# Performance work log

Measured on AMD Instinct MI355X. Metric: run time of the kernel, lower is better.

## Reference

```python
import jax, jax.numpy as jnp
import numpy as np

N_WIRES = 6
DIM = 1 << N_WIRES  # 64, equals input channel dim C for amplitude encoding
HID = N_WIRES       # hidden_dim = len(ops)


def _rx(theta):
    c = jnp.cos(theta / 2).astype(jnp.complex64)
    s = jnp.sin(theta / 2).astype(jnp.complex64)
    return jnp.stack([jnp.stack([c, -1j * s]), jnp.stack([-1j * s, c])])


def _ry(theta):
    c = jnp.cos(theta / 2).astype(jnp.complex64)
    s = jnp.sin(theta / 2).astype(jnp.complex64)
    return jnp.stack([jnp.stack([c, -s]), jnp.stack([s, c])])


def _apply_1q(state, U, wire):
    # state: (N, 2, 2, ..., 2); apply 2x2 U on qubit axis wire+1
    s = jnp.moveaxis(state, wire + 1, 1)
    s = jnp.einsum('ab,nb...->na...', U, s)
    return jnp.moveaxis(s, 1, wire + 1)


def _apply_cnot(state, c, t):
    # flip target axis where control bit == 1
    s = jnp.moveaxis(state, (c + 1, t + 1), (1, 2))
    s = jnp.concatenate([s[:, :1], jnp.flip(s[:, 1:2], axis=2)], axis=1)
    return jnp.moveaxis(s, (1, 2), (c + 1, t + 1))


def _expval_z(state, wire):
    # <Z_wire> = P(bit=0) - P(bit=1)
    p = state.real ** 2 + state.imag ** 2
    p = jnp.moveaxis(p, wire + 1, 1).reshape(p.shape[0], 2, -1)
    return p[:, 0].sum(-1) - p[:, 1].sum(-1)


def _value_layer(x_flat, params, qk):
    # amplitude encoding: normalize input into state amplitudes (C == DIM)
    norm = jnp.linalg.norm(x_flat, axis=-1, keepdims=True)
    psi = (x_flat / norm).astype(jnp.complex64)
    state = psi.reshape((x_flat.shape[0],) + (2,) * N_WIRES)
    rx0, ry0, ry1 = params[0], params[1], params[2]
    for j in range(N_WIRES):
        state = _apply_1q(state, _rx(rx0[j]), j)
        state = _apply_1q(state, _ry(ry0[j]), j)
    for j in range(N_WIRES):
        state = _apply_cnot(state, j, (j + 1) % N_WIRES)
    for j in range(N_WIRES):
        state = _apply_1q(state, _ry(ry1[j]), j)
    if qk:
        z0 = _expval_z(state, 0)
        return jnp.stack([z0] * HID, axis=-1)  # qk=True replicates wire-0 <Z>
    return jnp.stack([_expval_z(state, w) for w in range(N_WIRES)], axis=-1)


def setup_inputs() -> dict:
    key = jax.random.key(0)
    k1, k2, k3, k4 = jax.random.split(key, 4)
    B, T, C = 16, 2048, DIM
    return {
        'x': jax.random.normal(k1, (B, T, C), dtype=jnp.float32),
        'params_q': jax.random.normal(k2, (3, N_WIRES), dtype=jnp.float32),
        'params_k': jax.random.normal(k3, (3, N_WIRES), dtype=jnp.float32),
        'params_v': jax.random.normal(k4, (3, N_WIRES), dtype=jnp.float32),
    }


def reference(x, params_q, params_k, params_v):
    B, T, C = x.shape
    xf = x.reshape(B * T, C)
    q = _value_layer(xf, params_q, True).reshape(B, T, HID)
    k = _value_layer(xf, params_k, True).reshape(B, T, HID)
    v = _value_layer(xf, params_v, False).reshape(B, T, HID)
    scores = jnp.einsum('btd,bsd->bts', q, k) / jnp.sqrt(jnp.float32(HID))
    attn = jax.nn.softmax(scores, axis=-1)
    return jnp.einsum('bts,bsd->btd', attn, v)
```

## Files before the change

### kernel.cpp

```cpp
#include <hip/hip_runtime.h>
#include <math.h>

#define NWIRES 6
#define DIM 64
#define NTOK 32768
#define NBATCH 16
#define TPB 2048
#define NMOM 16
#define SQRT6F 2.4494897427831781f
#define APAD 76

typedef short bf16x8 __attribute__((ext_vector_type(8)));
typedef float f32x4  __attribute__((ext_vector_type(4)));

__device__ __forceinline__ unsigned f2bfbits(float f) {
    unsigned u = __float_as_uint(f);
    return (u + 0x7FFF + ((u >> 16) & 1)) >> 16;
}
__device__ __forceinline__ float bfbits2f(unsigned b) {
    return __uint_as_float(b << 16);
}
__device__ __forceinline__ float pswap(float v) { return __shfl_xor(v, 1, 64); }

__global__ __attribute__((amdgpu_waves_per_eu(1, 4)))
__launch_bounds__(256) void qsa_sim(
        const float* __restrict__ x,
        const float* __restrict__ pq,
        const float* __restrict__ pk,
        const float* __restrict__ pv,
        float* __restrict__ zq,
        float* __restrict__ kv) {
    __shared__ unsigned short sAh[128 * APAD];
    __shared__ unsigned short sAl[128 * APAD];
    __shared__ float sTc[64], sTs[64], sP[24];
    int tid = threadIdx.x;
    int tbase = blockIdx.x * 256;
    int circ = blockIdx.y;
    const float* p = (circ == 0) ? pq : (circ == 1 ? pk : pv);

    int lane = tid & 63, wv = tid >> 6;
    int q4 = lane >> 4, c16 = lane & 15;
    int mytok0 = wv * 64 + 0 * 16 + c16;
    const float* xr0 = x + ((size_t)(tbase + mytok0)) * 64;
    float4 rw[4];
#pragma unroll
    for (int ks = 0; ks < 2; ++ks) {
        rw[ks * 2 + 0] = *(const float4*)(xr0 + ks * 32 + q4 * 8);
        rw[ks * 2 + 1] = *(const float4*)(xr0 + ks * 32 + q4 * 8 + 4);
    }

    if (tid < 64) {
        int b = tid;
        float d = 0.f;
#pragma unroll
        for (int j = 0; j < 6; ++j)
            d += 0.5f * p[j] * ((b & (32 >> j)) ? -1.f : 1.f);
        float sd, cd;
        sincosf(d, &sd, &cd);
        sTc[b] = cd;
        sTs[b] = sd;
        if (b < 12) {
            float s, cc;
            sincosf(0.5f * p[6 + b], &s, &cc);
            sP[b * 2 + 0] = cc;
            sP[b * 2 + 1] = s;
        }
    }
    __syncthreads();

    {
        int ph = tid >> 7;
        int k  = (tid >> 1) & 63;
        int h  = tid & 1;
        const float* sTx = ph ? sTs : sTc;
        float v[32];
#pragma unroll
        for (int i = 0; i < 32; ++i) {
            int g = h * 32 + i;
            v[i] = (__popc(g & k) & 1) ? -sTx[g] : sTx[g];
        }
#pragma unroll
        for (int i = 0; i < 32; ++i) {
            float pv_ = pswap(v[i]);
            v[i] = h ? (pv_ - v[i]) : (v[i] + pv_);
        }
#pragma unroll
        for (int M = 16; M >= 1; M >>= 1) {
#pragma unroll
            for (int i = 0; i < 32; ++i) {
                if (i & M) continue;
                int j = i | M;
                float a = v[i], b = v[j];
                v[i] = a + b; v[j] = a - b;
            }
        }
#pragma unroll
        for (int layer = 0; layer < 2; ++layer) {
            const float* Pl = sP + layer * 12;
            {
                float c = Pl[0], ss = h ? Pl[1] : -Pl[1];
#pragma unroll
                for (int i = 0; i < 32; ++i) {
                    float pv_ = pswap(v[i]);
                    v[i] = c * v[i] + ss * pv_;
                }
            }
#pragma unroll
            for (int w = 1; w < 6; ++w) {
                int M = 32 >> w;
                float c = Pl[w * 2], s = Pl[w * 2 + 1];
#pragma unroll
                for (int i = 0; i < 32; ++i) {
                    if (i & M) continue;
                    int j = i | M;
                    float a = v[i], b = v[j];
                    v[i] = c * a - s * b;
                    v[j] = s * a + c * b;
                }
            }
            if (layer == 0) {
#pragma unroll
                for (int i = 0; i < 16; ++i) {
                    int j = i | 16;
                    float a = v[i], b = v[j];
                    v[i] = h ? b : a;
                    v[j] = h ? a : b;
                }
#pragma unroll
                for (int w = 1; w < 5; ++w) {
                    int MC = 32 >> w, MT = MC >> 1;
#pragma unroll
                    for (int i = 0; i < 32; ++i) {
                        if (!(i & MC) || (i & MT)) continue;
                        int j = i | MT;
                        float t = v[i]; v[i] = v[j]; v[j] = t;
                    }
                }
#pragma unroll
                for (int i = 1; i < 32; i += 2) v[i] = pswap(v[i]);
            }
        }
#pragma unroll
        for (int i = 0; i < 32; ++i) {
            int row = ph * 64 + h * 32 + i;
            unsigned hb = f2bfbits(v[i]);
            unsigned lb = f2bfbits(v[i] - bfbits2f(hb));
            sAh[row * APAD + k] = (unsigned short)hb;
            sAl[row * APAD + k] = (unsigned short)lb;
        }
    }
    __syncthreads();

    bf16x8 xh[2], xl[2];
#pragma unroll 1
    for (int cg = 0; cg < 4; ++cg) {
#pragma unroll
        for (int ks = 0; ks < 2; ++ks) {
            float4 f0 = rw[ks * 2], f1 = rw[ks * 2 + 1];
            float ff[8] = {f0.x, f0.y, f0.z, f0.w, f1.x, f1.y, f1.z, f1.w};
#pragma unroll
            for (int e = 0; e < 8; ++e) {
                unsigned hb = f2bfbits(ff[e]);
                unsigned lb = f2bfbits(ff[e] - bfbits2f(hb));
                xh[ks][e] = (short)hb;
                xl[ks][e] = (short)lb;
            }
        }
        int mytok = wv * 64 + cg * 16 + c16;
        if (cg < 3) {
            const float* xrn = x + ((size_t)(tbase + mytok + 16)) * 64;
#pragma unroll
            for (int ks = 0; ks < 2; ++ks) {
                rw[ks * 2 + 0] = *(const float4*)(xrn + ks * 32 + q4 * 8);
                rw[ks * 2 + 1] = *(const float4*)(xrn + ks * 32 + q4 * 8 + 4);
            }
        }

        f32x4 acc[8];
#pragma unroll
        for (int mt = 0; mt < 8; ++mt) acc[mt] = (f32x4){0.f, 0.f, 0.f, 0.f};
#pragma unroll
        for (int mt = 0; mt < 8; ++mt) {
            int r = mt * 16 + c16;
#pragma unroll
            for (int ks = 0; ks < 2; ++ks) {
                const uint2* ph_ = (const uint2*)(&sAh[r * APAD + ks * 32 + q4 * 8]);
                const uint2* pl_ = (const uint2*)(&sAl[r * APAD + ks * 32 + q4 * 8]);
                union { uint2 u[2]; bf16x8 v; } ua, ub;
                ua.u[0] = ph_[0]; ua.u[1] = ph_[1];
                ub.u[0] = pl_[0]; ub.u[1] = pl_[1];
                bf16x8 ah = ua.v, al = ub.v;
                acc[mt] = __builtin_amdgcn_mfma_f32_16x16x32_bf16(ah, xh[ks], acc[mt], 0, 0, 0);
                acc[mt] = __builtin_amdgcn_mfma_f32_16x16x32_bf16(ah, xl[ks], acc[mt], 0, 0, 0);
                acc[mt] = __builtin_amdgcn_mfma_f32_16x16x32_bf16(al, xh[ks], acc[mt], 0, 0, 0);
            }
        }

        float n = 0.f, s0 = 0.f, s1 = 0.f, s2 = 0.f, s3 = 0.f, s4 = 0.f, s5 = 0.f;
        float f2 = (q4 < 2) ? 1.f : 0.f;
        float f3 = (q4 & 1) ? 0.f : 1.f;
#pragma unroll
        for (int mt = 0; mt < 4; ++mt) {
#pragma unroll
            for (int rg = 0; rg < 4; ++rg) {
                float dc = acc[mt][rg];
                float ds = acc[mt + 4][rg];
                float pp = dc * dc + ds * ds;
                n += pp;
                if (!(mt & 2)) s0 += pp;
                if (!(mt & 1)) s1 += pp;
                s2 += f2 * pp;
                s3 += f3 * pp;
                if (!(rg & 2)) s4 += pp;
                if (!(rg & 1)) s5 += pp;
            }
        }
#pragma unroll
        for (int d = 16; d <= 32; d <<= 1) {
            n  += __shfl_xor(n,  d, 64);
            s0 += __shfl_xor(s0, d, 64);
            s1 += __shfl_xor(s1, d, 64);
            s2 += __shfl_xor(s2, d, 64);
            s3 += __shfl_xor(s3, d, 64);
            s4 += __shfl_xor(s4, d, 64);
            s5 += __shfl_xor(s5, d, 64);
        }
        if (q4 == 0) {
            int t = tbase + mytok;
            float inv = 1.0f / n;
            if (circ == 0) {
                zq[t] = SQRT6F * (2.f * s0 - n) * inv;
            } else if (circ == 1) {
                kv[(size_t)t * 8] = (2.f * s0 - n) * inv;
            } else {
                float* o = kv + (size_t)t * 8;
                o[1] = (2.f*s0 - n) * inv;
                o[2] = (2.f*s1 - n) * inv;
                o[3] = (2.f*s2 - n) * inv;
                o[4] = (2.f*s3 - n) * inv;
                o[5] = (2.f*s4 - n) * inv;
                o[6] = (2.f*s5 - n) * inv;
                o[7] = 0.f;
            }
        }
    }
}

__global__ __attribute__((amdgpu_waves_per_eu(1, 2)))
__launch_bounds__(64) void qsa_moments_partial(
        const float* __restrict__ kv,
        float* __restrict__ mpart) {
    int blk = blockIdx.x;
    int b = blk >> 3, c = blk & 7;
    int lane = threadIdx.x;
    float S[NMOM], H[NMOM][6];
#pragma unroll
    for (int m = 0; m < NMOM; ++m) {
        S[m] = 0.f;
#pragma unroll
        for (int w = 0; w < 6; ++w) H[m][w] = 0.f;
    }
    const float* base = kv + ((size_t)(b * TPB + c * 256)) * 8;
#pragma unroll
    for (int r = 0; r < 4; ++r) {
        const float4* e = (const float4*)(base + (size_t)(r * 64 + lane) * 8);
        float4 e0 = e[0], e1 = e[1];
        float z = e0.x;
        float v0 = e0.y, v1 = e0.z, v2 = e0.w, v3 = e1.x, v4 = e1.y, v5 = e1.z;
        float pw = 1.f;
#pragma unroll
        for (int m = 0; m < NMOM; ++m) {
            S[m] += pw;
            H[m][0] += pw * v0; H[m][1] += pw * v1; H[m][2] += pw * v2;
            H[m][3] += pw * v3; H[m][4] += pw * v4; H[m][5] += pw * v5;
            pw *= z;
        }
    }
#pragma unroll
    for (int d = 32; d >= 1; d >>= 1) {
#pragma unroll
        for (int m = 0; m < NMOM; ++m) {
            S[m] += __shfl_xor(S[m], d, 64);
#pragma unroll
            for (int w = 0; w < 6; ++w) H[m][w] += __shfl_xor(H[m][w], d, 64);
        }
    }
    if (lane == 0) {
        float* o = mpart + (size_t)blk * 112;
#pragma unroll
        for (int m = 0; m < NMOM; ++m) {
            float* om = o + m * 7;
            om[0] = S[m];
            om[1] = H[m][0]; om[2] = H[m][1]; om[3] = H[m][2];
            om[4] = H[m][3]; om[5] = H[m][4]; om[6] = H[m][5];
        }
    }
}

__global__ __launch_bounds__(256) void qsa_eval(
        const float* __restrict__ zq,
        const float* __restrict__ mpart,
        float* __restrict__ out) {
    __shared__ float sm[112];
    int bk = blockIdx.x;
    int b = bk >> 3;
    int tid = threadIdx.x;
    if (tid < 112) {
        float s = 0.f;
#pragma unroll
        for (int c = 0; c < 8; ++c) s += mpart[(size_t)(b * 8 + c) * 112 + tid];
        sm[tid] = s;
    }
    __syncthreads();

    int t = bk * 256 + tid;
    float a = zq[t];
    float den = 0.f, o0 = 0.f, o1 = 0.f, o2 = 0.f, o3 = 0.f, o4 = 0.f, o5 = 0.f;
    float pw = 1.f;
#pragma unroll
    for (int m = 0; m < NMOM; ++m) {
        const float* mm = sm + m * 7;
        den += pw * mm[0];
        o0 += pw * mm[1]; o1 += pw * mm[2]; o2 += pw * mm[3];
        o3 += pw * mm[4]; o4 += pw * mm[5]; o5 += pw * mm[6];
        pw *= a * (1.0f / (m + 1));
    }
    float inv = 1.0f / den;
    float* o = out + (size_t)t * 6;
    float2* o2p = (float2*)o;
    o2p[0] = make_float2(o0 * inv, o1 * inv);
    o2p[1] = make_float2(o2 * inv, o3 * inv);
    o2p[2] = make_float2(o4 * inv, o5 * inv);
}

extern "C" void kernel_launch(void* const* d_in, const int* in_sizes, int n_in,
                              void* d_out, int out_size, void* d_ws, size_t ws_size,
                              hipStream_t stream) {
    const float* x  = (const float*)d_in[0];
    const float* pq = (const float*)d_in[1];
    const float* pk = (const float*)d_in[2];
    const float* pv = (const float*)d_in[3];
    float* w = (float*)d_ws;
    float* zq    = w;
    float* kv    = zq + NTOK;
    float* mpart = kv + NTOK * 8;
    float* out   = (float*)d_out;

    qsa_sim<<<dim3(NTOK / 256, 3), 256, 0, stream>>>(x, pq, pk, pv, zq, kv);
    qsa_moments_partial<<<NBATCH * 8, 64, 0, stream>>>(kv, mpart);
    qsa_eval<<<NTOK / 256, 256, 0, stream>>>(zq, mpart, out);
}
```

Before: 85.44 us.

## Fuse moment reduction into simulation kernel and keep K/V in shared memory

Merges the moments-partial kernel into the simulation kernel. K and V blocks now process both circuits for 128 tokens, keep their expectation values in shared memory and reduce Taylor moments in place. This drops one launch and the global kv round-trip. Blocks become 128 tokens, so there are 16 partial chunks per batch, and the K/V blocks run two sequential A-builds and MFMA passes. That creates imbalance against the Q-only blocks.

```diff
diff --git a/kernel.cpp b/kernel.cpp
--- a/kernel.cpp
+++ b/kernel.cpp
@@ -5,7 +5,6 @@
 #define DIM 64
 #define NTOK 32768
 #define NBATCH 16
-#define TPB 2048
 #define NMOM 16
 #define SQRT6F 2.4494897427831781f
 #define APAD 76
@@ -22,33 +21,11 @@
 }
 __device__ __forceinline__ float pswap(float v) { return __shfl_xor(v, 1, 64); }
 
-__global__ __attribute__((amdgpu_waves_per_eu(1, 4)))
-__launch_bounds__(256) void qsa_sim(
-        const float* __restrict__ x,
-        const float* __restrict__ pq,
-        const float* __restrict__ pk,
-        const float* __restrict__ pv,
-        float* __restrict__ zq,
-        float* __restrict__ kv) {
-    __shared__ unsigned short sAh[128 * APAD];
-    __shared__ unsigned short sAl[128 * APAD];
-    __shared__ float sTc[64], sTs[64], sP[24];
-    int tid = threadIdx.x;
-    int tbase = blockIdx.x * 256;
-    int circ = blockIdx.y;
-    const float* p = (circ == 0) ? pq : (circ == 1 ? pk : pv);
-
-    int lane = tid & 63, wv = tid >> 6;
-    int q4 = lane >> 4, c16 = lane & 15;
-    int mytok0 = wv * 64 + 0 * 16 + c16;
-    const float* xr0 = x + ((size_t)(tbase + mytok0)) * 64;
-    float4 rw[4];
-#pragma unroll
-    for (int ks = 0; ks < 2; ++ks) {
-        rw[ks * 2 + 0] = *(const float4*)(xr0 + ks * 32 + q4 * 8);
-        rw[ks * 2 + 1] = *(const float4*)(xr0 + ks * 32 + q4 * 8 + 4);
-    }
-
+__device__ __forceinline__ void build_A(
+        int tid, const float* __restrict__ p,
+        float* sTc, float* sTs, float* sP,
+        unsigned short* sAh, unsigned short* sAl) {
+    __syncthreads();
     if (tid < 64) {
         int b = tid;
         float d = 0.f;
@@ -68,92 +45,109 @@
     }
     __syncthreads();
 
-    {
-        int ph = tid >> 7;
-        int k  = (tid >> 1) & 63;
-        int h  = tid & 1;
-        const float* sTx = ph ? sTs : sTc;
-        float v[32];
+    int ph = tid >> 7;
+    int k  = (tid >> 1) & 63;
+    int h  = tid & 1;
+    const float* sTx = ph ? sTs : sTc;
+    float v[32];
+#pragma unroll
+    for (int i = 0; i < 32; ++i) {
+        int g = h * 32 + i;
+        v[i] = (__popc(g & k) & 1) ? -sTx[g] : sTx[g];
+    }
+#pragma unroll
+    for (int i = 0; i < 32; ++i) {
+        float pv_ = pswap(v[i]);
+        v[i] = h ? (pv_ - v[i]) : (v[i] + pv_);
+    }
+#pragma unroll
+    for (int M = 16; M >= 1; M >>= 1) {
 #pragma unroll
         for (int i = 0; i < 32; ++i) {
-            int g = h * 32 + i;
-            v[i] = (__popc(g & k) & 1) ? -sTx[g] : sTx[g];
-        }
-#pragma unroll
-        for (int i = 0; i < 32; ++i) {
-            float pv_ = pswap(v[i]);
-            v[i] = h ? (pv_ - v[i]) : (v[i] + pv_);
-        }
-#pragma unroll
-        for (int M = 16; M >= 1; M >>= 1) {
+            if (i & M) continue;
+            int j = i | M;
+            float a = v[i], b = v[j];
+            v[i] = a + b; v[j] = a - b;
+        }
+    }
+#pragma unroll
+    for (int layer = 0; layer < 2; ++layer) {
+        const float* Pl = sP + layer * 12;
+        {
+            float c = Pl[0], ss = h ? Pl[1] : -Pl[1];
+#pragma unroll
+            for (int i = 0; i < 32; ++i) {
+                float pv_ = pswap(v[i]);
+                v[i] = c * v[i] + ss * pv_;
+            }
+        }
+#pragma unroll
+        for (int w = 1; w < 6; ++w) {
+            int M = 32 >> w;
+            float c = Pl[w * 2], s = Pl[w * 2 + 1];
 #pragma unroll
             for (int i = 0; i < 32; ++i) {
                 if (i & M) continue;
                 int j = i | M;
                 float a = v[i], b = v[j];
-                v[i] = a + b; v[j] = a - b;
-            }
-        }
-#pragma unroll
-        for (int layer = 0; layer < 2; ++layer) {
-            const float* Pl = sP + layer * 12;
-            {
-                float c = Pl[0], ss = h ? Pl[1] : -Pl[1];
+                v[i] = c * a - s * b;
+                v[j] = s * a + c * b;
+            }
+        }
+        if (layer == 0) {
+#pragma unroll
+            for (int i = 0; i < 16; ++i) {
+                int j = i | 16;
+                float a = v[i], b = v[j];
+                v[i] = h ? b : a;
+                v[j] = h ? a : b;
+            }
+#pragma unroll
+            for (int w = 1; w < 5; ++w) {
+                int MC = 32 >> w, MT = MC >> 1;
 #pragma unroll
                 for (int i = 0; i < 32; ++i) {
-                    float pv_ = pswap(v[i]);
-                    v[i] = c * v[i] + ss * pv_;
+                    if (!(i & MC) || (i & MT)) continue;
+                    int j = i | MT;
+                    float t = v[i]; v[i] = v[j]; v[j] = t;
                 }
             }
 #pragma unroll
-            for (int w = 1; w < 6; ++w) {
-                int M = 32 >> w;
-                float c = Pl[w * 2], s = Pl[w * 2 + 1];
-#pragma unroll
-                for (int i = 0; i < 32; ++i) {
-                    if (i & M) continue;
-                    int j = i | M;
-                    float a = v[i], b = v[j];
-                    v[i] = c * a - s * b;
-                    v[j] = s * a + c * b;
-                }
-            }
-            if (layer == 0) {
-#pragma unroll
-                for (int i = 0; i < 16; ++i) {
-                    int j = i | 16;
-                    float a = v[i], b = v[j];
-                    v[i] = h ? b : a;
-                    v[j] = h ? a : b;
-                }
-#pragma unroll
-                for (int w = 1; w < 5; ++w) {
-                    int MC = 32 >> w, MT = MC >> 1;
-#pragma unroll
-                    for (int i = 0; i < 32; ++i) {
-                        if (!(i & MC) || (i & MT)) continue;
-                        int j = i | MT;
-                        float t = v[i]; v[i] = v[j]; v[j] = t;
-                    }
-                }
-#pragma unroll
-                for (int i = 1; i < 32; i += 2) v[i] = pswap(v[i]);
-            }
-        }
-#pragma unroll
-        for (int i = 0; i < 32; ++i) {
-            int row = ph * 64 + h * 32 + i;
-            unsigned hb = f2bfbits(v[i]);
-            unsigned lb = f2bfbits(v[i] - bfbits2f(hb));
-            sAh[row * APAD + k] = (unsigned short)hb;
-            sAl[row * APAD + k] = (unsigned short)lb;
-        }
-    }
-    __syncthreads();
+            for (int i = 1; i < 32; i += 2) v[i] = pswap(v[i]);
+        }
+    }
+#pragma unroll
+    for (int i = 0; i < 32; ++i) {
+        int row = ph * 64 + h * 32 + i;
+        unsigned hb = f2bfbits(v[i]);
+        unsigned lb = f2bfbits(v[i] - bfbits2f(hb));
+        sAh[row * APAD + k] = (unsigned short)hb;
+        sAl[row * APAD + k] = (unsigned short)lb;
+    }
+    __syncthreads();
+}
+
+template<int MODE>
+__device__ __forceinline__ void mfma_pass(
+        int tid, const float* __restrict__ x, int tbase,
+        const unsigned short* sAh, const unsigned short* sAl,
+        float* __restrict__ zq, float* zkv) {
+    int lane = tid & 63, wv = tid >> 6;
+    int q4 = lane >> 4, c16 = lane & 15;
+
+    float4 rw[4];
+    {
+        const float* xr0 = x + ((size_t)(tbase + wv * 32 + c16)) * 64;
+#pragma unroll
+        for (int ks = 0; ks < 2; ++ks) {
+            rw[ks * 2 + 0] = *(const float4*)(xr0 + ks * 32 + q4 * 8);
+            rw[ks * 2 + 1] = *(const float4*)(xr0 + ks * 32 + q4 * 8 + 4);
+        }
+    }
 
     bf16x8 xh[2], xl[2];
 #pragma unroll 1
-    for (int cg = 0; cg < 4; ++cg) {
+    for (int cg = 0; cg < 2; ++cg) {
 #pragma unroll
         for (int ks = 0; ks < 2; ++ks) {
             float4 f0 = rw[ks * 2], f1 = rw[ks * 2 + 1];
@@ -166,8 +160,8 @@
                 xl[ks][e] = (short)lb;
             }
         }
-        int mytok = wv * 64 + cg * 16 + c16;
-        if (cg < 3) {
+        int mytok = wv * 32 + cg * 16 + c16;
+        if (cg < 1) {
             const float* xrn = x + ((size_t)(tbase + mytok + 16)) * 64;
 #pragma unroll
             for (int ks = 0; ks < 2; ++ks) {
@@ -226,74 +220,98 @@
             s5 += __shfl_xor(s5, d, 64);
         }
         if (q4 == 0) {
-            int t = tbase + mytok;
             float inv = 1.0f / n;
-            if (circ == 0) {
-                zq[t] = SQRT6F * (2.f * s0 - n) * inv;
-            } else if (circ == 1) {
-                kv[(size_t)t * 8] = (2.f * s0 - n) * inv;
+            if (MODE == 0) {
+                zq[tbase + mytok] = SQRT6F * (2.f * s0 - n) * inv;
+            } else if (MODE == 1) {
+                zkv[mytok * 8] = (2.f * s0 - n) * inv;
             } else {
-                float* o = kv + (size_t)t * 8;
+                float* o = zkv + mytok * 8;
                 o[1] = (2.f*s0 - n) * inv;
                 o[2] = (2.f*s1 - n) * inv;
                 o[3] = (2.f*s2 - n) * inv;
                 o[4] = (2.f*s3 - n) * inv;
                 o[5] = (2.f*s4 - n) * inv;
                 o[6] = (2.f*s5 - n) * inv;
-                o[7] = 0.f;
-            }
-        }
-    }
-}
-
-__global__ __attribute__((amdgpu_waves_per_eu(1, 2)))
-__launch_bounds__(64) void qsa_moments_partial(
-        const float* __restrict__ kv,
+            }
+        }
+    }
+}
+
+__global__ __attribute__((amdgpu_waves_per_eu(1, 4)))
+__launch_bounds__(256) void qsa_sim(
+        const float* __restrict__ x,
+        const float* __restrict__ pq,
+        const float* __restrict__ pk,
+        const float* __restrict__ pv,
+        float* __restrict__ zq,
         float* __restrict__ mpart) {
-    int blk = blockIdx.x;
-    int b = blk >> 3, c = blk & 7;
-    int lane = threadIdx.x;
-    float S[NMOM], H[NMOM][6];
-#pragma unroll
-    for (int m = 0; m < NMOM; ++m) {
-        S[m] = 0.f;
-#pragma unroll
-        for (int w = 0; w < 6; ++w) H[m][w] = 0.f;
-    }
-    const float* base = kv + ((size_t)(b * TPB + c * 256)) * 8;
-#pragma unroll
-    for (int r = 0; r < 4; ++r) {
-        const float4* e = (const float4*)(base + (size_t)(r * 64 + lane) * 8);
-        float4 e0 = e[0], e1 = e[1];
-        float z = e0.x;
-        float v0 = e0.y, v1 = e0.z, v2 = e0.w, v3 = e1.x, v4 = e1.y, v5 = e1.z;
-        float pw = 1.f;
-#pragma unroll
-        for (int m = 0; m < NMOM; ++m) {
-            S[m] += pw;
-            H[m][0] += pw * v0; H[m][1] += pw * v1; H[m][2] += pw * v2;
-            H[m][3] += pw * v3; H[m][4] += pw * v4; H[m][5] += pw * v5;
+    __shared__ unsigned short sAh[128 * APAD];
+    __shared__ unsigned short sAl[128 * APAD];
+    __shared__ float sTc[64], sTs[64], sP[24];
+    __shared__ float zkv[128 * 8];
+    __shared__ float smom[4][56];
+    int tid = threadIdx.x;
+    int bid = blockIdx.x;
+
+    if (bid < 256) {
+        int tbase = bid * 128;
+        build_A(tid, pq, sTc, sTs, sP, sAh, sAl);
+        mfma_pass<0>(tid, x, tbase, sAh, sAl, zq, zkv);
+        return;
+    }
+
+    int cc = bid - 256;
+    int tbase = cc * 128;
+    build_A(tid, pk, sTc, sTs, sP, sAh, sAl);
+    mfma_pass<1>(tid, x, tbase, sAh, sAl, zq, zkv);
+    build_A(tid, pv, sTc, sTs, sP, sAh, sAl);
+    mfma_pass<2>(tid, x, tbase, sAh, sAl, zq, zkv);
+    __syncthreads();
+
+    {
+        int t = tid & 127;
+        int half = tid >> 7;
+        int wv = tid >> 6, lane = tid & 63;
+        const float* e = zkv + t * 8;
+        float z = e[0];
+        float v0 = e[1], v1 = e[2], v2 = e[3], v3 = e[4], v4 = e[5], v5 = e[6];
+        float pw;
+        if (half) { float z2 = z * z; float z4 = z2 * z2; pw = z4 * z4; }
+        else pw = 1.f;
+        float S[8], H[8][6];
+#pragma unroll
+        for (int m = 0; m < 8; ++m) {
+            S[m] = pw;
+            H[m][0] = pw * v0; H[m][1] = pw * v1; H[m][2] = pw * v2;
+            H[m][3] = pw * v3; H[m][4] = pw * v4; H[m][5] = pw * v5;
             pw *= z;
         }
-    }
-#pragma unroll
-    for (int d = 32; d >= 1; d >>= 1) {
-#pragma unroll
-        for (int m = 0; m < NMOM; ++m) {
-            S[m] += __shfl_xor(S[m], d, 64);
-#pragma unroll
-            for (int w = 0; w < 6; ++w) H[m][w] += __shfl_xor(H[m][w], d, 64);
-        }
-    }
-    if (lane == 0) {
-        float* o = mpart + (size_t)blk * 112;
-#pragma unroll
-        for (int m = 0; m < NMOM; ++m) {
-            float* om = o + m * 7;
-            om[0] = S[m];
-            om[1] = H[m][0]; om[2] = H[m][1]; om[3] = H[m][2];
-            om[4] = H[m][3]; om[5] = H[m][4]; om[6] = H[m][5];
-        }
+#pragma unroll
+        for (int d = 32; d >= 1; d >>= 1) {
+#pragma unroll
+            for (int m = 0; m < 8; ++m) {
+                S[m] += __shfl_xor(S[m], d, 64);
+#pragma unroll
+                for (int w = 0; w < 6; ++w) H[m][w] += __shfl_xor(H[m][w], d, 64);
+            }
+        }
+        if (lane == 0) {
+#pragma unroll
+            for (int m = 0; m < 8; ++m) {
+                smom[wv][m * 7 + 0] = S[m];
+#pragma unroll
+                for (int w = 0; w < 6; ++w) smom[wv][m * 7 + 1 + w] = H[m][w];
+            }
+        }
+    }
+    __syncthreads();
+    if (tid < 112) {
+        int m = tid / 7, comp = tid % 7;
+        int half = m >> 3, ml = m & 7;
+        float val = smom[half * 2 + 0][ml * 7 + comp]
+                  + smom[half * 2 + 1][ml * 7 + comp];
+        mpart[(size_t)cc * 112 + tid] = val;
     }
 }
 
@@ -308,7 +326,8 @@
     if (tid < 112) {
         float s = 0.f;
 #pragma unroll
-        for (int c = 0; c < 8; ++c) s += mpart[(size_t)(b * 8 + c) * 112 + tid];
+        for (int c = 0; c < 16; ++c)
+            s += mpart[(size_t)(b * 16 + c) * 112 + tid];
         sm[tid] = s;
     }
     __syncthreads();
@@ -342,11 +361,9 @@
     const float* pv = (const float*)d_in[3];
     float* w = (float*)d_ws;
     float* zq    = w;
-    float* kv    = zq + NTOK;
-    float* mpart = kv + NTOK * 8;
+    float* mpart = zq + NTOK;
     float* out   = (float*)d_out;
 
-    qsa_sim<<<dim3(NTOK / 256, 3), 256, 0, stream>>>(x, pq, pk, pv, zq, kv);
-    qsa_moments_partial<<<NBATCH * 8, 64, 0, stream>>>(kv, mpart);
+    qsa_sim<<<512, 256, 0, stream>>>(x, pq, pk, pv, zq, mpart);
     qsa_eval<<<NTOK / 256, 256, 0, stream>>>(zq, mpart, out);
 }
```

Result: no change. 85.55 us (+0.1%).
